# Kernel optimization log

Measured on AMD Instinct MI355X. Metric: run time of the kernel, lower is better.

Reference implementation:

```python
import jax, jax.numpy as jnp
import numpy as np

# Physical constants (normalized units, CFL-stable: c*dt/dx = 0.5)
DX = 0.01
DT = 0.005
C = 1.0
EPSILON = 1.0

def _make_kernels():
    # D02: second derivative along last axis (x); D20 = transpose (y)
    d02 = np.array([[0.0, 0.0, 0.0],
                    [1.0, -2.0, 1.0],
                    [0.0, 0.0, 0.0]], dtype=np.float32) / (DX * DX)
    d20 = d02.T
    # OIHW, single in/out channel
    return jnp.asarray(d02)[None, None], jnp.asarray(d20)[None, None]

_D02, _D20 = _make_kernels()

def _conv3x3(u, k):
    # same padding, stride 1, NCHW
    return jax.lax.conv_general_dilated(
        u, k, window_strides=(1, 1), padding=[(1, 1), (1, 1)],
        dimension_numbers=('NCHW', 'OIHW', 'NCHW'))

def setup_inputs() -> dict:
    key = jax.random.key(0)
    k1, k2, k3, k4 = jax.random.split(key, 4)
    B, H, W = 16, 1024, 1024
    shp = (B, 1, H, W)
    return {
        'u1': jax.random.normal(k1, shp, dtype=jnp.float32),
        'u0': jax.random.normal(k2, shp, dtype=jnp.float32),
        'j2': jax.random.normal(k3, shp, dtype=jnp.float32),
        'j0': jax.random.normal(k4, shp, dtype=jnp.float32),
    }

def reference(u1, u0, j2, j0):
    D20u1 = _conv3x3(u1, _D20)  # d^2/dy^2
    D02u1 = _conv3x3(u1, _D02)  # d^2/dx^2
    u2 = (2.0 * u1 - u0
          + (DT * DT) * (C * C) * (D20u1 + D02u1)
          - (DT / (2.0 * EPSILON)) * (j2 - j0))
    return u2
```

## Files before the change

### kernel.cpp

```cpp
#include <hip/hip_runtime.h>

#define WIDTH  1024
#define HEIGHT 1024
#define R      4

typedef float vfloat4 __attribute__((ext_vector_type(4)));

__global__ __launch_bounds__(256) void fdtd_kernel(
    const float* __restrict__ u1,
    const float* __restrict__ u0,
    const float* __restrict__ j2,
    const float* __restrict__ j0,
    float* __restrict__ out,
    int chunk)
{
    const int bid = blockIdx.x;
    const int swz = chunk ? ((bid & 7) * chunk + (bid >> 3)) : bid;

    const int y0 = swz * R;
    const int iy = y0 & (HEIGHT - 1);
    const int x0 = threadIdx.x << 2;
    const long base = (long)y0 * WIDTH + x0;
    const vfloat4 zero = {0.f, 0.f, 0.f, 0.f};

    vfloat4 c[R + 2];
    c[0] = (iy > 0) ? *(const vfloat4*)(u1 + base - WIDTH) : zero;
#pragma unroll
    for (int r = 0; r < R; ++r)
        c[r + 1] = *(const vfloat4*)(u1 + base + (long)r * WIDTH);
    c[R + 1] = (iy + R < HEIGHT) ? *(const vfloat4*)(u1 + base + (long)R * WIDTH) : zero;

    float lf[R], rt[R];
#pragma unroll
    for (int r = 0; r < R; ++r) {
        lf[r] = (x0 > 0)         ? u1[base + (long)r * WIDTH - 1] : 0.f;
        rt[r] = (x0 + 4 < WIDTH) ? u1[base + (long)r * WIDTH + 4] : 0.f;
    }

    vfloat4 a0[R], v2[R], v0[R];
#pragma unroll
    for (int r = 0; r < R; ++r) {
        const long b = base + (long)r * WIDTH;
        a0[r] = *(const vfloat4*)(u0 + b);
        v2[r] = *(const vfloat4*)(j2 + b);
        v0[r] = *(const vfloat4*)(j0 + b);
    }

#pragma unroll
    for (int r = 0; r < R; ++r) {
        const vfloat4 up = c[r], ce = c[r + 1], dn = c[r + 2];
        vfloat4 o;
        o.x = 2.0f * ce.x - a0[r].x + 0.25f * (up.x + dn.x + lf[r] + ce.y - 4.0f * ce.x)
            - 0.0025f * (v2[r].x - v0[r].x);
        o.y = 2.0f * ce.y - a0[r].y + 0.25f * (up.y + dn.y + ce.x + ce.z - 4.0f * ce.y)
            - 0.0025f * (v2[r].y - v0[r].y);
        o.z = 2.0f * ce.z - a0[r].z + 0.25f * (up.z + dn.z + ce.y + ce.w - 4.0f * ce.z)
            - 0.0025f * (v2[r].z - v0[r].z);
        o.w = 2.0f * ce.w - a0[r].w + 0.25f * (up.w + dn.w + ce.z + rt[r] - 4.0f * ce.w)
            - 0.0025f * (v2[r].w - v0[r].w);
        *(vfloat4*)(out + base + (long)r * WIDTH) = o;
    }
}

extern "C" void kernel_launch(void* const* d_in, const int* in_sizes, int n_in,
                              void* d_out, int out_size, void* d_ws, size_t ws_size,
                              hipStream_t stream) {
    const float* u1 = (const float*)d_in[0];
    const float* u0 = (const float*)d_in[1];
    const float* j2 = (const float*)d_in[2];
    const float* j0 = (const float*)d_in[3];
    float* out = (float*)d_out;

    const int nrows   = out_size / WIDTH;
    const int nblocks = nrows / R;
    const int chunk   = (nblocks % 8 == 0) ? (nblocks >> 3) : 0;

    dim3 block(WIDTH / 4);
    dim3 grid(nblocks);
    fdtd_kernel<<<grid, block, 0, stream>>>(u1, u0, j2, j0, out, chunk);
}
```

Before: 264.2 us.

## Stream rows through register window with prefetch, shuffles, and nontemporal access

Each block now walks 8 rows using a rolling three-row register window, prefetching the next row's inputs one step ahead. Horizontal neighbours come from wave shuffles instead of extra scalar global loads, with only wave-edge lanes loading from memory. Loads and stores of single-use streams use nontemporal hints, and launch bounds request higher occupancy. The shallower in-flight load depth may reduce memory-level parallelism compared with issuing all rows' loads at once.

```diff
diff --git a/kernel.cpp b/kernel.cpp
--- a/kernel.cpp
+++ b/kernel.cpp
@@ -2,11 +2,11 @@
 
 #define WIDTH  1024
 #define HEIGHT 1024
-#define R      4
+#define WALK   8
 
 typedef float vfloat4 __attribute__((ext_vector_type(4)));
 
-__global__ __launch_bounds__(256) void fdtd_kernel(
+__global__ __launch_bounds__(256, 4) void fdtd_kernel(
     const float* __restrict__ u1,
     const float* __restrict__ u0,
     const float* __restrict__ j2,
@@ -17,48 +17,60 @@
     const int bid = blockIdx.x;
     const int swz = chunk ? ((bid & 7) * chunk + (bid >> 3)) : bid;
 
-    const int y0 = swz * R;
-    const int iy = y0 & (HEIGHT - 1);
-    const int x0 = threadIdx.x << 2;
+    const int y0   = swz * WALK;
+    const int iy   = y0 & (HEIGHT - 1);
+    const int x0   = threadIdx.x << 2;
+    const int lane = threadIdx.x & 63;
     const long base = (long)y0 * WIDTH + x0;
     const vfloat4 zero = {0.f, 0.f, 0.f, 0.f};
 
-    vfloat4 c[R + 2];
-    c[0] = (iy > 0) ? *(const vfloat4*)(u1 + base - WIDTH) : zero;
-#pragma unroll
-    for (int r = 0; r < R; ++r)
-        c[r + 1] = *(const vfloat4*)(u1 + base + (long)r * WIDTH);
-    c[R + 1] = (iy + R < HEIGHT) ? *(const vfloat4*)(u1 + base + (long)R * WIDTH) : zero;
+    vfloat4 w0, w1, w2;
+    w0 = (iy > 0) ? *(const vfloat4*)(u1 + base - WIDTH) : zero;
+    w1 = *(const vfloat4*)(u1 + base);
+    w2 = *(const vfloat4*)(u1 + base + WIDTH);
 
-    float lf[R], rt[R];
-#pragma unroll
-    for (int r = 0; r < R; ++r) {
-        lf[r] = (x0 > 0)         ? u1[base + (long)r * WIDTH - 1] : 0.f;
-        rt[r] = (x0 + 4 < WIDTH) ? u1[base + (long)r * WIDTH + 4] : 0.f;
-    }
-
-    vfloat4 a0[R], v2[R], v0[R];
-#pragma unroll
-    for (int r = 0; r < R; ++r) {
-        const long b = base + (long)r * WIDTH;
-        a0[r] = *(const vfloat4*)(u0 + b);
-        v2[r] = *(const vfloat4*)(j2 + b);
-        v0[r] = *(const vfloat4*)(j0 + b);
-    }
+    vfloat4 a0b[2], v2b[2], v0b[2];
+    float   elb[2], erb[2];
+    a0b[0] = __builtin_nontemporal_load((const vfloat4*)(u0 + base));
+    v2b[0] = __builtin_nontemporal_load((const vfloat4*)(j2 + base));
+    v0b[0] = __builtin_nontemporal_load((const vfloat4*)(j0 + base));
+    elb[0] = (lane == 0  && x0 > 0)         ? u1[base - 1] : 0.f;
+    erb[0] = (lane == 63 && x0 + 4 < WIDTH) ? u1[base + 4] : 0.f;
 
 #pragma unroll
-    for (int r = 0; r < R; ++r) {
-        const vfloat4 up = c[r], ce = c[r + 1], dn = c[r + 2];
+    for (int s = 0; s < WALK; ++s) {
+        const int cur = s & 1, nxt = cur ^ 1;
+
+        vfloat4 nx = zero;
+        if (s + 1 < WALK) {
+            const long bn = base + (long)(s + 1) * WIDTH;
+            a0b[nxt] = __builtin_nontemporal_load((const vfloat4*)(u0 + bn));
+            v2b[nxt] = __builtin_nontemporal_load((const vfloat4*)(j2 + bn));
+            v0b[nxt] = __builtin_nontemporal_load((const vfloat4*)(j0 + bn));
+            elb[nxt] = (lane == 0  && x0 > 0)         ? u1[bn - 1] : 0.f;
+            erb[nxt] = (lane == 63 && x0 + 4 < WIDTH) ? u1[bn + 4] : 0.f;
+            if (s + 2 < WALK || iy + WALK < HEIGHT)
+                nx = *(const vfloat4*)(u1 + base + (long)(s + 2) * WIDTH);
+        }
+
+        float lf = __shfl_up(w1.w, 1);
+        if (lane == 0)  lf = elb[cur];
+        float rt = __shfl_down(w1.x, 1);
+        if (lane == 63) rt = erb[cur];
+
+        const vfloat4 a0 = a0b[cur], v2 = v2b[cur], v0 = v0b[cur];
         vfloat4 o;
-        o.x = 2.0f * ce.x - a0[r].x + 0.25f * (up.x + dn.x + lf[r] + ce.y - 4.0f * ce.x)
-            - 0.0025f * (v2[r].x - v0[r].x);
-        o.y = 2.0f * ce.y - a0[r].y + 0.25f * (up.y + dn.y + ce.x + ce.z - 4.0f * ce.y)
-            - 0.0025f * (v2[r].y - v0[r].y);
-        o.z = 2.0f * ce.z - a0[r].z + 0.25f * (up.z + dn.z + ce.y + ce.w - 4.0f * ce.z)
-            - 0.0025f * (v2[r].z - v0[r].z);
-        o.w = 2.0f * ce.w - a0[r].w + 0.25f * (up.w + dn.w + ce.z + rt[r] - 4.0f * ce.w)
-            - 0.0025f * (v2[r].w - v0[r].w);
-        *(vfloat4*)(out + base + (long)r * WIDTH) = o;
+        o.x = 2.0f * w1.x - a0.x + 0.25f * (w0.x + w2.x + lf   + w1.y - 4.0f * w1.x)
+            - 0.0025f * (v2.x - v0.x);
+        o.y = 2.0f * w1.y - a0.y + 0.25f * (w0.y + w2.y + w1.x + w1.z - 4.0f * w1.y)
+            - 0.0025f * (v2.y - v0.y);
+        o.z = 2.0f * w1.z - a0.z + 0.25f * (w0.z + w2.z + w1.y + w1.w - 4.0f * w1.z)
+            - 0.0025f * (v2.z - v0.z);
+        o.w = 2.0f * w1.w - a0.w + 0.25f * (w0.w + w2.w + w1.z + rt   - 4.0f * w1.w)
+            - 0.0025f * (v2.w - v0.w);
+        __builtin_nontemporal_store(o, (vfloat4*)(out + base + (long)s * WIDTH));
+
+        w0 = w1; w1 = w2; w2 = nx;
     }
 }
 
@@ -72,7 +84,7 @@
     float* out = (float*)d_out;
 
     const int nrows   = out_size / WIDTH;
-    const int nblocks = nrows / R;
+    const int nblocks = nrows / WALK;
     const int chunk   = (nblocks % 8 == 0) ? (nblocks >> 3) : 0;
 
     dim3 block(WIDTH / 4);
```

Result: faster. 258.5 us (-2.2%).

## Stage inputs via direct global-to-LDS loads, shrink rows per block, nontemporal stores

Applied to the files above, without the earlier changes.

Each block now handles 2 rows instead of 4 and copies the needed u1 halo rows plus the u0/j2/j0 rows straight into LDS with global_load_lds. It then computes the stencil from LDS, taking left and right neighbours from LDS rather than issuing scalar global loads. Output is written with nontemporal stores. The aims are to drop redundant unaligned halo loads and to raise memory-level parallelism. The cost is a 40KB LDS footprint per block, which limits occupancy, a block barrier, and more vertical halo re-reads per output row because each block covers fewer rows.

```diff
diff --git a/kernel.cpp b/kernel.cpp
--- a/kernel.cpp
+++ b/kernel.cpp
@@ -2,9 +2,11 @@
 
 #define WIDTH  1024
 #define HEIGHT 1024
-#define R      4
+#define R      2
 
 typedef float vfloat4 __attribute__((ext_vector_type(4)));
+typedef __attribute__((address_space(3))) void       lds_void;
+typedef __attribute__((address_space(1))) const void gbl_void;
 
 __global__ __launch_bounds__(256) void fdtd_kernel(
     const float* __restrict__ u1,
@@ -14,51 +16,74 @@
     float* __restrict__ out,
     int chunk)
 {
+    __shared__ float lds[10 * WIDTH];
+
     const int bid = blockIdx.x;
     const int swz = chunk ? ((bid & 7) * chunk + (bid >> 3)) : bid;
 
-    const int y0 = swz * R;
-    const int iy = y0 & (HEIGHT - 1);
-    const int x0 = threadIdx.x << 2;
-    const long base = (long)y0 * WIDTH + x0;
-    const vfloat4 zero = {0.f, 0.f, 0.f, 0.f};
+    const int y0  = swz * R;
+    const int iy  = y0 & (HEIGHT - 1);
+    const int tid = threadIdx.x;
+    const int wid = tid >> 6;
+    const long base = (long)y0 * WIDTH;
 
-    vfloat4 c[R + 2];
-    c[0] = (iy > 0) ? *(const vfloat4*)(u1 + base - WIDTH) : zero;
-#pragma unroll
-    for (int r = 0; r < R; ++r)
-        c[r + 1] = *(const vfloat4*)(u1 + base + (long)r * WIDTH);
-    c[R + 1] = (iy + R < HEIGHT) ? *(const vfloat4*)(u1 + base + (long)R * WIDTH) : zero;
+    const long  upRow  = (iy > 0)          ? base - WIDTH            : base;
+    const long  dnRow  = (iy + R < HEIGHT) ? base + (long)R * WIDTH  : base + (long)(R - 1) * WIDTH;
+    const float upMask = (iy > 0)          ? 1.0f : 0.0f;
+    const float dnMask = (iy + R < HEIGHT) ? 1.0f : 0.0f;
 
-    float lf[R], rt[R];
-#pragma unroll
-    for (int r = 0; r < R; ++r) {
-        lf[r] = (x0 > 0)         ? u1[base + (long)r * WIDTH - 1] : 0.f;
-        rt[r] = (x0 + 4 < WIDTH) ? u1[base + (long)r * WIDTH + 4] : 0.f;
-    }
+    const int goff = tid << 2;
+    float* const lwave = lds + (wid << 8);
 
-    vfloat4 a0[R], v2[R], v0[R];
-#pragma unroll
-    for (int r = 0; r < R; ++r) {
-        const long b = base + (long)r * WIDTH;
-        a0[r] = *(const vfloat4*)(u0 + b);
-        v2[r] = *(const vfloat4*)(j2 + b);
-        v0[r] = *(const vfloat4*)(j0 + b);
-    }
+    #define STAGE(grow, lrow)                                                       \
+        __builtin_amdgcn_global_load_lds((gbl_void*)((grow) + goff),                \
+                                         (lds_void*)(lwave + (lrow) * WIDTH),       \
+                                         16, 0, 0)
+    STAGE(u1 + upRow,        0);
+    STAGE(u1 + base,         1);
+    STAGE(u1 + base + WIDTH, 2);
+    STAGE(u1 + dnRow,        3);
+    STAGE(u0 + base,         4);
+    STAGE(u0 + base + WIDTH, 5);
+    STAGE(j2 + base,         6);
+    STAGE(j2 + base + WIDTH, 7);
+    STAGE(j0 + base,         8);
+    STAGE(j0 + base + WIDTH, 9);
+    #undef STAGE
+
+    __syncthreads();
+
+    const int   x0     = tid << 2;
+    const int   lfi    = (x0 > 0)         ? x0 - 1 : 0;
+    const int   rti    = (x0 + 4 < WIDTH) ? x0 + 4 : WIDTH - 1;
+    const float lfMask = (x0 > 0)         ? 1.0f : 0.0f;
+    const float rtMask = (x0 + 4 < WIDTH) ? 1.0f : 0.0f;
 
 #pragma unroll
     for (int r = 0; r < R; ++r) {
-        const vfloat4 up = c[r], ce = c[r + 1], dn = c[r + 2];
+        vfloat4 up = *(const vfloat4*)(lds + (r    ) * WIDTH + x0);
+        vfloat4 ce = *(const vfloat4*)(lds + (r + 1) * WIDTH + x0);
+        vfloat4 dn = *(const vfloat4*)(lds + (r + 2) * WIDTH + x0);
+        if (r == 0)     up *= upMask;
+        if (r == R - 1) dn *= dnMask;
+
+        const float lfv = lds[(r + 1) * WIDTH + lfi] * lfMask;
+        const float rtv = lds[(r + 1) * WIDTH + rti] * rtMask;
+
+        const vfloat4 a0 = *(const vfloat4*)(lds + (4 + r) * WIDTH + x0);
+        const vfloat4 v2 = *(const vfloat4*)(lds + (6 + r) * WIDTH + x0);
+        const vfloat4 v0 = *(const vfloat4*)(lds + (8 + r) * WIDTH + x0);
+
         vfloat4 o;
-        o.x = 2.0f * ce.x - a0[r].x + 0.25f * (up.x + dn.x + lf[r] + ce.y - 4.0f * ce.x)
-            - 0.0025f * (v2[r].x - v0[r].x);
-        o.y = 2.0f * ce.y - a0[r].y + 0.25f * (up.y + dn.y + ce.x + ce.z - 4.0f * ce.y)
-            - 0.0025f * (v2[r].y - v0[r].y);
-        o.z = 2.0f * ce.z - a0[r].z + 0.25f * (up.z + dn.z + ce.y + ce.w - 4.0f * ce.z)
-            - 0.0025f * (v2[r].z - v0[r].z);
-        o.w = 2.0f * ce.w - a0[r].w + 0.25f * (up.w + dn.w + ce.z + rt[r] - 4.0f * ce.w)
-            - 0.0025f * (v2[r].w - v0[r].w);
-        *(vfloat4*)(out + base + (long)r * WIDTH) = o;
+        o.x = 2.0f * ce.x - a0.x + 0.25f * (up.x + dn.x + lfv  + ce.y - 4.0f * ce.x)
+            - 0.0025f * (v2.x - v0.x);
+        o.y = 2.0f * ce.y - a0.y + 0.25f * (up.y + dn.y + ce.x + ce.z - 4.0f * ce.y)
+            - 0.0025f * (v2.y - v0.y);
+        o.z = 2.0f * ce.z - a0.z + 0.25f * (up.z + dn.z + ce.y + ce.w - 4.0f * ce.z)
+            - 0.0025f * (v2.z - v0.z);
+        o.w = 2.0f * ce.w - a0.w + 0.25f * (up.w + dn.w + ce.z + rtv  - 4.0f * ce.w)
+            - 0.0025f * (v2.w - v0.w);
+        __builtin_nontemporal_store(o, (vfloat4*)(out + base + (long)r * WIDTH + x0));
     }
 }
 
```

New measurement: 260.1 us. Within noise of the previous version (-1.6%).
